# Kernel tuning notes

Measured on AMD Instinct MI355X. Metric: run time of the kernel, lower is better.

The kernel has to match this reference:

```python
import jax, jax.numpy as jnp
import numpy as np

N = 2000      # batch_size * num_rois
PS = 7        # pool_size
C = 256       # roi-align channels
HID = 1024    # head width
NC = 81       # num_classes (COCO incl. background)
EPS = 1e-3    # keras BatchNormalization default epsilon


def setup_inputs() -> dict:
    key = jax.random.key(0)
    ks = jax.random.split(key, 6)
    sc = lambda k, shape, s: jax.random.normal(k, shape, jnp.float32) * s
    return {
        "pooled_rois": jax.random.normal(ks[0], (N, PS, PS, C), jnp.float32),
        # 7x7 VALID conv on a 7x7 input == flattened dense: [PS*PS*C, HID]
        "w1": sc(ks[1], (PS * PS * C, HID), 0.01),
        "b1": jnp.zeros((HID,), jnp.float32),
        "gamma1": jnp.ones((HID,), jnp.float32),
        "beta1": jnp.zeros((HID,), jnp.float32),
        # 1x1 conv == dense [HID, HID]
        "w2": sc(ks[2], (HID, HID), 0.02),
        "b2": jnp.zeros((HID,), jnp.float32),
        "gamma2": jnp.ones((HID,), jnp.float32),
        "beta2": jnp.zeros((HID,), jnp.float32),
        "w_logits": sc(ks[3], (HID, NC), 0.02),
        "b_logits": jnp.zeros((NC,), jnp.float32),
        "w_delta": sc(ks[4], (HID, NC * 4), 0.02),
        "b_delta": jnp.zeros((NC * 4,), jnp.float32),
    }


def _batchnorm_train(x, gamma, beta):
    # training=True: normalize with batch statistics over the RoI axis
    mu = jnp.mean(x, axis=0)
    var = jnp.var(x, axis=0)
    return gamma * (x - mu) * jax.lax.rsqrt(var + EPS) + beta


def reference(pooled_rois, w1, b1, gamma1, beta1, w2, b2, gamma2, beta2,
              w_logits, b_logits, w_delta, b_delta):
    n = pooled_rois.shape[0]
    # rcnn_class_conv1: 7x7 VALID conv on 7x7 input -> flatten + matmul
    x = pooled_rois.reshape(n, -1) @ w1 + b1          # [N, 1024]
    x = jax.nn.relu(_batchnorm_train(x, gamma1, beta1))
    # rcnn_class_conv2: 1x1 conv -> matmul
    x = x @ w2 + b2                                    # [N, 1024]
    x = jax.nn.relu(_batchnorm_train(x, gamma2, beta2))
    logits = x @ w_logits + b_logits                   # [N, NC]
    probs = jax.nn.softmax(logits, axis=-1)            # [N, NC]
    deltas = (x @ w_delta + b_delta).reshape(n, NC, 4) # [N, NC, 4]
    return logits, probs, deltas
```

## Files before the change

kernel.cpp:

```cpp
#include <hip/hip_runtime.h>

typedef unsigned short u16;
typedef __bf16 bf16x8 __attribute__((ext_vector_type(8)));
typedef float f32x4 __attribute__((ext_vector_type(4)));
typedef u16 u16x8 __attribute__((ext_vector_type(8)));
typedef u16 u16x4 __attribute__((ext_vector_type(4)));

static constexpr int kNRoi = 2000;
static constexpr int kMPad = 2048;
static constexpr int kKin  = 12544;
static constexpr int kHid  = 1024;
static constexpr int kNOutPad = 512;
static constexpr int kNC = 81;
static constexpr int kND = 324;

__device__ __forceinline__ float bf2f(u16 h) {
  union { unsigned u; float f; } v; v.u = ((unsigned)h) << 16; return v.f;
}
__device__ __forceinline__ u16 f2bf(float f) {
  union { float f; unsigned u; } v; v.f = f;
  unsigned r = v.u + 0x7fffu + ((v.u >> 16) & 1u);
  return (u16)(r >> 16);
}

__global__ void sniff(const void* __restrict__ g, int* __restrict__ flag) {
  *flag = (((const unsigned*)g)[0] == 0x3f800000u) ? 1 : 0;
}

__global__ void to_bf16(const void* __restrict__ in, u16* __restrict__ out,
                        const int* __restrict__ flagp) {
  const int f32 = *flagp;
  long i = ((long)blockIdx.x * blockDim.x + threadIdx.x) * 8;
  u16x8 h;
  if (f32) {
    f32x4 a = *(const f32x4*)((const float*)in + i);
    f32x4 b = *(const f32x4*)((const float*)in + i + 4);
#pragma unroll
    for (int j = 0; j < 4; ++j) { h[j] = f2bf(a[j]); h[4 + j] = f2bf(b[j]); }
  } else {
    h = *(const u16x8*)((const u16*)in + i);
  }
  *(u16x8*)(out + i) = h;
}

__global__ void transpose_fast(const void* __restrict__ in, u16* __restrict__ out,
                               int R, int C, const int* __restrict__ flagp) {
  __shared__ u16 t[64 * 72];
  const int f32 = *flagp;
  const int tid = threadIdx.x;
  const int cb = blockIdx.x * 64, rb = blockIdx.y * 64;
  const int rl = tid >> 4;
  const int cl = (tid & 15) * 4;
#pragma unroll
  for (int i = 0; i < 4; ++i) {
    int r = rl + i * 16;
    long idx = (long)(rb + r) * C + cb + cl;
    u16 h[4];
    if (f32) {
      f32x4 v = *(const f32x4*)((const float*)in + idx);
#pragma unroll
      for (int j = 0; j < 4; ++j) h[j] = f2bf(v[j]);
    } else {
      u16x4 v = *(const u16x4*)((const u16*)in + idx);
#pragma unroll
      for (int j = 0; j < 4; ++j) h[j] = v[j];
    }
#pragma unroll
    for (int j = 0; j < 4; ++j) t[(cl + j) * 72 + r] = h[j];
  }
  __syncthreads();
  const int c2 = tid >> 3;
  const int r2 = (tid & 7) * 8;
#pragma unroll
  for (int i = 0; i < 2; ++i) {
    int c = c2 + i * 32;
    u16x8 v = *(const u16x8*)&t[c * 72 + r2];
    *(u16x8*)(out + (long)(cb + c) * R + rb + r2) = v;
  }
}

__global__ void transpose_any(const void* __restrict__ in, u16* __restrict__ out,
                              int R, int C, const int* __restrict__ flagp) {
  __shared__ u16 t[32][33];
  const int f32 = *flagp;
  int tx = threadIdx.x & 31, ty = threadIdx.x >> 5;
  int cb = blockIdx.x * 32, rb = blockIdx.y * 32;
#pragma unroll
  for (int i = 0; i < 4; ++i) {
    int r = rb + ty + i * 8, c = cb + tx;
    if (r < R && c < C) {
      long idx = (long)r * C + c;
      t[ty + i * 8][tx] = f32 ? f2bf(((const float*)in)[idx]) : ((const u16*)in)[idx];
    }
  }
  __syncthreads();
#pragma unroll
  for (int i = 0; i < 4; ++i) {
    int c = cb + ty + i * 8, r = rb + tx;
    if (c < C && r < R) out[(long)c * R + r] = t[tx][ty + i * 8];
  }
}

__global__ __launch_bounds__(256) void gemm_bt(
    const u16* __restrict__ A, const u16* __restrict__ Bt,
    float* __restrict__ C, int Mreal, int K, int N, int kchunk) {
  __shared__ u16 As[2][128 * 32];
  __shared__ u16 Bs[2][128 * 32];
  const int tid  = threadIdx.x;
  const int lane = tid & 63;
  const int wave = tid >> 6;
  const int wm = (wave >> 1) * 64;
  const int wn = (wave & 1) * 64;

  f32x4 acc[4][4] = {};

  const int r0 = tid >> 2;
  const int kc = (tid & 3) * 8;
  long ar0 = (long)blockIdx.x * 128 + r0;      if (ar0 > Mreal - 1) ar0 = Mreal - 1;
  long ar1 = (long)blockIdx.x * 128 + 64 + r0; if (ar1 > Mreal - 1) ar1 = Mreal - 1;
  const long br0 = (long)blockIdx.y * 128 + r0;
  const long br1 = br0 + 64;

  const int kb = blockIdx.z * kchunk;
  const u16* ag0 = A + ar0 * K + kb + kc;
  const u16* ag1 = A + ar1 * K + kb + kc;
  const u16* bg0 = Bt + br0 * K + kb + kc;
  const u16* bg1 = Bt + br1 * K + kb + kc;

  const int fr = lane & 15;
  const int fq = (lane >> 4) * 8;
  const int iters = kchunk / 32;

#define STAGE(b) do {                                                          \
    u16* al_ = As[b] + wave * 512;                                             \
    u16* bl_ = Bs[b] + wave * 512;                                             \
    __builtin_amdgcn_global_load_lds((const __attribute__((address_space(1))) void*)ag0, \
                                     (__attribute__((address_space(3))) void*)al_, 16, 0, 0); \
    __builtin_amdgcn_global_load_lds((const __attribute__((address_space(1))) void*)ag1, \
                                     (__attribute__((address_space(3))) void*)(al_ + 2048), 16, 0, 0); \
    __builtin_amdgcn_global_load_lds((const __attribute__((address_space(1))) void*)bg0, \
                                     (__attribute__((address_space(3))) void*)bl_, 16, 0, 0); \
    __builtin_amdgcn_global_load_lds((const __attribute__((address_space(1))) void*)bg1, \
                                     (__attribute__((address_space(3))) void*)(bl_ + 2048), 16, 0, 0); \
    ag0 += 32; ag1 += 32; bg0 += 32; bg1 += 32;                                \
  } while (0)

  STAGE(0);
  int buf = 0;
  for (int it = 0; it < iters; ++it) {
    __syncthreads();
    if (it + 1 < iters) STAGE(buf ^ 1);

    const u16* as_ = As[buf];
    const u16* bs_ = Bs[buf];
    bf16x8 afr[4], bfr[4];
#pragma unroll
    for (int i = 0; i < 4; ++i)
      afr[i] = *(const bf16x8*)(as_ + (wm + i * 16 + fr) * 32 + fq);
#pragma unroll
    for (int i = 0; i < 4; ++i)
      bfr[i] = *(const bf16x8*)(bs_ + (wn + i * 16 + fr) * 32 + fq);
#pragma unroll
    for (int mi = 0; mi < 4; ++mi)
#pragma unroll
      for (int ni = 0; ni < 4; ++ni)
        acc[mi][ni] = __builtin_amdgcn_mfma_f32_16x16x32_bf16(afr[mi], bfr[ni], acc[mi][ni], 0, 0, 0);
    buf ^= 1;
  }
#undef STAGE

  const int row0 = blockIdx.x * 128 + wm + (lane >> 4) * 4;
  const int col0 = blockIdx.y * 128 + wn + fr;
#pragma unroll
  for (int mi = 0; mi < 4; ++mi)
#pragma unroll
    for (int ni = 0; ni < 4; ++ni)
#pragma unroll
      for (int e = 0; e < 4; ++e)
        atomicAdd(&C[(long)(row0 + mi * 16 + e) * N + col0 + ni * 16], acc[mi][ni][e]);
}

__global__ void colstats(const float* __restrict__ X, float* __restrict__ S,
                         float* __restrict__ SS, int cols, int chunk) {
  int c = blockIdx.x * blockDim.x + threadIdx.x;
  int r0 = blockIdx.y * chunk;
  float s = 0.f, ss = 0.f;
  for (int r = r0; r < r0 + chunk; ++r) {
    float v = X[(long)r * cols + c];
    s += v; ss += v * v;
  }
  atomicAdd(&S[c], s);
  atomicAdd(&SS[c], ss);
}

__global__ void finalize_stats(const float* __restrict__ S, const float* __restrict__ SS,
                               const void* __restrict__ gamma, const void* __restrict__ beta,
                               float* __restrict__ SV, float* __restrict__ TV,
                               int n, float invN, const int* __restrict__ flagp) {
  const int f32 = *flagp;
  int c = blockIdx.x * blockDim.x + threadIdx.x;
  if (c < n) {
    float g = f32 ? ((const float*)gamma)[c] : bf2f(((const u16*)gamma)[c]);
    float b = f32 ? ((const float*)beta)[c]  : bf2f(((const u16*)beta)[c]);
    float mu = S[c] * invN;
    float var = SS[c] * invN - mu * mu;
    float sc = g * rsqrtf(var + 1e-3f);
    SV[c] = sc;
    TV[c] = b - mu * sc;
  }
}

__global__ void bn_relu_kernel(const float* __restrict__ X, const float* __restrict__ SV,
                               const float* __restrict__ TV, u16* __restrict__ H) {
  long i = ((long)blockIdx.x * blockDim.x + threadIdx.x) * 8;
  int c = (int)(i & (kHid - 1));
  f32x4 x0 = *(const f32x4*)(X + i);
  f32x4 x1 = *(const f32x4*)(X + i + 4);
  f32x4 s0 = *(const f32x4*)(SV + c);
  f32x4 s1 = *(const f32x4*)(SV + c + 4);
  f32x4 t0 = *(const f32x4*)(TV + c);
  f32x4 t1 = *(const f32x4*)(TV + c + 4);
  u16x8 h;
#pragma unroll
  for (int j = 0; j < 4; ++j) {
    h[j]     = f2bf(fmaxf(0.f, s0[j] * x0[j] + t0[j]));
    h[4 + j] = f2bf(fmaxf(0.f, s1[j] * x1[j] + t1[j]));
  }
  *(u16x8*)(H + i) = h;
}

__global__ void head_out(const float* __restrict__ X, const void* __restrict__ blv,
                         const void* __restrict__ bdv, void* __restrict__ outv,
                         const int* __restrict__ flagp) {
  const int f32 = *flagp;
  int lane = threadIdx.x & 63;
  int row = blockIdx.x * 4 + (threadIdx.x >> 6);
  if (row >= kNRoi) return;
  const float* xr = X + (long)row * kNOutPad;
  auto ldb = [&](const void* p, int i) -> float {
    return f32 ? ((const float*)p)[i] : bf2f(((const u16*)p)[i]);
  };
  auto st = [&](long i, float v) {
    if (f32) ((float*)outv)[i] = v; else ((u16*)outv)[i] = f2bf(v);
  };
  float v0 = xr[lane] + ldb(blv, lane);
  float v1 = (lane < kNC - 64) ? xr[64 + lane] + ldb(blv, 64 + lane) : -3.0e38f;
  float m = fmaxf(v0, v1);
#pragma unroll
  for (int off = 32; off > 0; off >>= 1) m = fmaxf(m, __shfl_xor(m, off, 64));
  float e0 = __expf(v0 - m);
  float e1 = (lane < kNC - 64) ? __expf(v1 - m) : 0.f;
  float s = e0 + e1;
#pragma unroll
  for (int off = 32; off > 0; off >>= 1) s += __shfl_xor(s, off, 64);
  float inv = 1.f / s;
  long lo = (long)row * kNC;
  long pr = (long)kNRoi * kNC + lo;
  long de = 2L * kNRoi * kNC + (long)row * kND;
  st(lo + lane, v0);
  st(pr + lane, e0 * inv);
  if (lane < kNC - 64) { st(lo + 64 + lane, v1); st(pr + 64 + lane, e1 * inv); }
#pragma unroll
  for (int j = 0; j < 5; ++j) {
    int c = lane + 64 * j;
    st(de + c, xr[kNC + c] + ldb(bdv, c));
  }
  if (lane < 4) { int c = lane + 320; st(de + c, xr[kNC + c] + ldb(bdv, c)); }
}

extern "C" void kernel_launch(void* const* d_in, const int* in_sizes, int n_in,
                              void* d_out, int out_size, void* d_ws, size_t ws_size,
                              hipStream_t stream) {
  const void* pooled   = d_in[0];
  const void* w1       = d_in[1];
  const void* gamma1   = d_in[3];
  const void* beta1    = d_in[4];
  const void* w2       = d_in[5];
  const void* gamma2   = d_in[7];
  const void* beta2    = d_in[8];
  const void* w_logits = d_in[9];
  const void* b_logits = d_in[10];
  const void* w_delta  = d_in[11];
  const void* b_delta  = d_in[12];

  char* ws = (char*)d_ws;
  u16*   W1T  = (u16*)(ws + 0);
  u16*   W2T  = (u16*)(ws + 25690112);
  u16*   WHT  = (u16*)(ws + 27787264);
  float* BUFA = (float*)(ws + 28835840);
  u16*   BUFB = (u16*)(ws + 37224448);
  float* S    = (float*)(ws + 41418752);
  float* SS   = S + 1024;
  float* SV   = S + 2048;
  float* TV   = S + 3072;
  int*   FLAG = (int*)(S + 4096);
  u16*   A1   = (u16*)(ws + 41451520);

  const float invN = 1.f / (float)kNRoi;

  sniff<<<1, 1, 0, stream>>>(gamma1, FLAG);

  to_bf16<<<12250, 256, 0, stream>>>(pooled, A1, FLAG);

  hipMemsetAsync(WHT, 0, (size_t)kNOutPad * kHid * sizeof(u16), stream);
  transpose_fast<<<dim3(16, 196), 256, 0, stream>>>(w1, W1T, kKin, kHid, FLAG);
  transpose_fast<<<dim3(16, 16),  256, 0, stream>>>(w2, W2T, kHid, kHid, FLAG);
  transpose_any<<<dim3(3, 32),   256, 0, stream>>>(w_logits, WHT, kHid, kNC, FLAG);
  transpose_any<<<dim3(11, 32),  256, 0, stream>>>(w_delta, WHT + (long)kNC * kHid, kHid, kND, FLAG);

  hipMemsetAsync(BUFA, 0, (size_t)kMPad * kHid * sizeof(float), stream);
  gemm_bt<<<dim3(16, 8, 8), 256, 0, stream>>>(A1, W1T, BUFA, kNRoi, kKin, kHid, kKin / 8);

  hipMemsetAsync(S, 0, 2 * kHid * sizeof(float), stream);
  colstats<<<dim3(kHid / 256, 80), 256, 0, stream>>>(BUFA, S, SS, kHid, kNRoi / 80);
  finalize_stats<<<kHid / 256, 256, 0, stream>>>(S, SS, gamma1, beta1, SV, TV, kHid, invN, FLAG);
  bn_relu_kernel<<<(kMPad * kHid) / (256 * 8), 256, 0, stream>>>(BUFA, SV, TV, BUFB);

  hipMemsetAsync(BUFA, 0, (size_t)kMPad * kHid * sizeof(float), stream);
  gemm_bt<<<dim3(16, 8, 2), 256, 0, stream>>>(BUFB, W2T, BUFA, kMPad, kHid, kHid, kHid / 2);

  hipMemsetAsync(S, 0, 2 * kHid * sizeof(float), stream);
  colstats<<<dim3(kHid / 256, 80), 256, 0, stream>>>(BUFA, S, SS, kHid, kNRoi / 80);
  finalize_stats<<<kHid / 256, 256, 0, stream>>>(S, SS, gamma2, beta2, SV, TV, kHid, invN, FLAG);
  bn_relu_kernel<<<(kMPad * kHid) / (256 * 8), 256, 0, stream>>>(BUFA, SV, TV, BUFB);

  hipMemsetAsync(BUFA, 0, (size_t)kMPad * kNOutPad * sizeof(float), stream);
  gemm_bt<<<dim3(16, 4, 4), 256, 0, stream>>>(BUFB, WHT, BUFA, kMPad, kHid, kNOutPad, kHid / 4);

  head_out<<<kNRoi / 4, 256, 0, stream>>>(BUFA, b_logits, b_delta, d_out, FLAG);
}
```

Before: 428.6 us.

## Fuse prep, zeroing and BN finalize kernels; drop dtype sniffing and memsets

All input conversion and weight transposes, plus zeroing of the accumulation buffers and stats, are merged into one prep kernel dispatched by block index. Zeroing of the second-layer and head output buffers is folded into the colstats kernel, and the BN scale/shift finalize is recomputed inline inside bn_relu. The runtime f32/bf16 sniff is removed and inputs are assumed to be f32. Split-K for the second GEMM goes from 2 to 4. The aim is to cut launch and memset overhead, at the cost of redundant per-element rsqrt work and more atomic traffic in GEMM2.

```diff
diff --git a/kernel.cpp b/kernel.cpp
--- a/kernel.cpp
+++ b/kernel.cpp
@@ -4,7 +4,6 @@
 typedef __bf16 bf16x8 __attribute__((ext_vector_type(8)));
 typedef float f32x4 __attribute__((ext_vector_type(4)));
 typedef u16 u16x8 __attribute__((ext_vector_type(8)));
-typedef u16 u16x4 __attribute__((ext_vector_type(4)));
 
 static constexpr int kNRoi = 2000;
 static constexpr int kMPad = 2048;
@@ -14,63 +13,27 @@
 static constexpr int kNC = 81;
 static constexpr int kND = 324;
 
-__device__ __forceinline__ float bf2f(u16 h) {
-  union { unsigned u; float f; } v; v.u = ((unsigned)h) << 16; return v.f;
-}
+
 __device__ __forceinline__ u16 f2bf(float f) {
   union { float f; unsigned u; } v; v.f = f;
   unsigned r = v.u + 0x7fffu + ((v.u >> 16) & 1u);
   return (u16)(r >> 16);
 }
 
-__global__ void sniff(const void* __restrict__ g, int* __restrict__ flag) {
-  *flag = (((const unsigned*)g)[0] == 0x3f800000u) ? 1 : 0;
-}
-
-__global__ void to_bf16(const void* __restrict__ in, u16* __restrict__ out,
-                        const int* __restrict__ flagp) {
-  const int f32 = *flagp;
-  long i = ((long)blockIdx.x * blockDim.x + threadIdx.x) * 8;
-  u16x8 h;
-  if (f32) {
-    f32x4 a = *(const f32x4*)((const float*)in + i);
-    f32x4 b = *(const f32x4*)((const float*)in + i + 4);
-#pragma unroll
-    for (int j = 0; j < 4; ++j) { h[j] = f2bf(a[j]); h[4 + j] = f2bf(b[j]); }
-  } else {
-    h = *(const u16x8*)((const u16*)in + i);
-  }
-  *(u16x8*)(out + i) = h;
-}
-
-__global__ void transpose_fast(const void* __restrict__ in, u16* __restrict__ out,
-                               int R, int C, const int* __restrict__ flagp) {
-  __shared__ u16 t[64 * 72];
-  const int f32 = *flagp;
-  const int tid = threadIdx.x;
-  const int cb = blockIdx.x * 64, rb = blockIdx.y * 64;
-  const int rl = tid >> 4;
-  const int cl = (tid & 15) * 4;
+__device__ __forceinline__ void transpose64(const float* __restrict__ in,
+                                            u16* __restrict__ out, int R, int C,
+                                            int bx, int by, u16* t, int tid) {
+  const int cb = bx * 64, rb = by * 64;
+  const int rl = tid >> 4, cl = (tid & 15) * 4;
 #pragma unroll
   for (int i = 0; i < 4; ++i) {
     int r = rl + i * 16;
-    long idx = (long)(rb + r) * C + cb + cl;
-    u16 h[4];
-    if (f32) {
-      f32x4 v = *(const f32x4*)((const float*)in + idx);
-#pragma unroll
-      for (int j = 0; j < 4; ++j) h[j] = f2bf(v[j]);
-    } else {
-      u16x4 v = *(const u16x4*)((const u16*)in + idx);
-#pragma unroll
-      for (int j = 0; j < 4; ++j) h[j] = v[j];
-    }
-#pragma unroll
-    for (int j = 0; j < 4; ++j) t[(cl + j) * 72 + r] = h[j];
+    f32x4 v = *(const f32x4*)(in + (long)(rb + r) * C + cb + cl);
+#pragma unroll
+    for (int j = 0; j < 4; ++j) t[(cl + j) * 72 + r] = f2bf(v[j]);
   }
   __syncthreads();
-  const int c2 = tid >> 3;
-  const int r2 = (tid & 7) * 8;
+  const int c2 = tid >> 3, r2 = (tid & 7) * 8;
 #pragma unroll
   for (int i = 0; i < 2; ++i) {
     int c = c2 + i * 32;
@@ -79,26 +42,64 @@
   }
 }
 
-__global__ void transpose_any(const void* __restrict__ in, u16* __restrict__ out,
-                              int R, int C, const int* __restrict__ flagp) {
-  __shared__ u16 t[32][33];
-  const int f32 = *flagp;
-  int tx = threadIdx.x & 31, ty = threadIdx.x >> 5;
-  int cb = blockIdx.x * 32, rb = blockIdx.y * 32;
+__device__ __forceinline__ void transpose32(const float* __restrict__ in,
+                                            u16* __restrict__ out, int R, int C,
+                                            int bx, int by, u16* t, int tid) {
+  int tx = tid & 31, ty = tid >> 5;
+  int cb = bx * 32, rb = by * 32;
 #pragma unroll
   for (int i = 0; i < 4; ++i) {
     int r = rb + ty + i * 8, c = cb + tx;
-    if (r < R && c < C) {
-      long idx = (long)r * C + c;
-      t[ty + i * 8][tx] = f32 ? f2bf(((const float*)in)[idx]) : ((const u16*)in)[idx];
-    }
+    if (r < R && c < C) t[(ty + i * 8) * 33 + tx] = f2bf(in[(long)r * C + c]);
   }
   __syncthreads();
 #pragma unroll
   for (int i = 0; i < 4; ++i) {
     int c = cb + ty + i * 8, r = rb + tx;
-    if (c < C && r < R) out[(long)c * R + r] = t[tx][ty + i * 8];
-  }
+    if (c < C && r < R) out[(long)c * R + r] = t[tx * 33 + ty + i * 8];
+  }
+}
+
+__global__ __launch_bounds__(256) void prep(
+    const float* __restrict__ pooled, const float* __restrict__ w1,
+    const float* __restrict__ w2, const float* __restrict__ wl,
+    const float* __restrict__ wd, u16* __restrict__ A1,
+    u16* __restrict__ W1T, u16* __restrict__ W2T, u16* __restrict__ WHT,
+    float* __restrict__ X1, float* __restrict__ S) {
+  __shared__ u16 sh[64 * 72];
+  const int tid = threadIdx.x;
+  int id = blockIdx.x;
+  if (id < 12250) {
+    long i = ((long)id * 256 + tid) * 8;
+    f32x4 a = *(const f32x4*)(pooled + i);
+    f32x4 b = *(const f32x4*)(pooled + i + 4);
+    u16x8 h;
+#pragma unroll
+    for (int j = 0; j < 4; ++j) { h[j] = f2bf(a[j]); h[4 + j] = f2bf(b[j]); }
+    *(u16x8*)(A1 + i) = h;
+    return;
+  }
+  id -= 12250;
+  if (id < 3136) { transpose64(w1, W1T, kKin, kHid, id & 15, id >> 4, sh, tid); return; }
+  id -= 3136;
+  if (id < 256)  { transpose64(w2, W2T, kHid, kHid, id & 15, id >> 4, sh, tid); return; }
+  id -= 256;
+  if (id < 96)   { transpose32(wl, WHT, kHid, kNC, id % 3, id / 3, sh, tid); return; }
+  id -= 96;
+  if (id < 352)  { transpose32(wd, WHT + kNC * kHid, kHid, kND, id % 11, id / 11, sh, tid); return; }
+  id -= 352;
+  if (id < 54) {
+    int idx = id * 256 + tid;
+    if (idx < 13696) *(u16x8*)(WHT + 405 * kHid + idx * 8) = (u16x8){};
+    return;
+  }
+  id -= 54;
+  if (id < 2048) {
+    *(f32x4*)(X1 + ((long)id * 256 + tid) * 4) = (f32x4){};
+    return;
+  }
+  id -= 2048;
+  *(f32x4*)(S + ((long)id * 256 + tid) * 4) = (f32x4){};
 }
 
 __global__ __launch_bounds__(256) void gemm_bt(
@@ -180,71 +181,63 @@
         atomicAdd(&C[(long)(row0 + mi * 16 + e) * N + col0 + ni * 16], acc[mi][ni][e]);
 }
 
-__global__ void colstats(const float* __restrict__ X, float* __restrict__ S,
-                         float* __restrict__ SS, int cols, int chunk) {
-  int c = blockIdx.x * blockDim.x + threadIdx.x;
-  int r0 = blockIdx.y * chunk;
-  float s = 0.f, ss = 0.f;
-  for (int r = r0; r < r0 + chunk; ++r) {
-    float v = X[(long)r * cols + c];
-    s += v; ss += v * v;
-  }
-  atomicAdd(&S[c], s);
-  atomicAdd(&SS[c], ss);
-}
-
-__global__ void finalize_stats(const float* __restrict__ S, const float* __restrict__ SS,
-                               const void* __restrict__ gamma, const void* __restrict__ beta,
-                               float* __restrict__ SV, float* __restrict__ TV,
-                               int n, float invN, const int* __restrict__ flagp) {
-  const int f32 = *flagp;
-  int c = blockIdx.x * blockDim.x + threadIdx.x;
-  if (c < n) {
-    float g = f32 ? ((const float*)gamma)[c] : bf2f(((const u16*)gamma)[c]);
-    float b = f32 ? ((const float*)beta)[c]  : bf2f(((const u16*)beta)[c]);
-    float mu = S[c] * invN;
-    float var = SS[c] * invN - mu * mu;
-    float sc = g * rsqrtf(var + 1e-3f);
-    SV[c] = sc;
-    TV[c] = b - mu * sc;
-  }
-}
-
-__global__ void bn_relu_kernel(const float* __restrict__ X, const float* __restrict__ SV,
-                               const float* __restrict__ TV, u16* __restrict__ H) {
-  long i = ((long)blockIdx.x * blockDim.x + threadIdx.x) * 8;
+__global__ __launch_bounds__(256) void colstats_zero(
+    const float* __restrict__ X, float* __restrict__ S, float* __restrict__ SS,
+    float* __restrict__ Z) {
+  int id = blockIdx.x;
+  if (id < 320) {
+    int c = (id & 3) * 256 + threadIdx.x;
+    int r0 = (id >> 2) * 25;
+    float s = 0.f, ss = 0.f;
+    for (int r = r0; r < r0 + 25; ++r) {
+      float v = X[(long)r * kHid + c];
+      s += v; ss += v * v;
+    }
+    atomicAdd(&S[c], s);
+    atomicAdd(&SS[c], ss);
+  } else {
+    id -= 320;
+    *(f32x4*)(Z + ((long)id * 256 + threadIdx.x) * 4) = (f32x4){};
+  }
+}
+
+__global__ __launch_bounds__(256) void bn_relu(
+    const float* __restrict__ X, const float* __restrict__ S,
+    const float* __restrict__ SS, const float* __restrict__ gamma,
+    const float* __restrict__ beta, u16* __restrict__ H) {
+  constexpr float invN = 1.f / (float)kNRoi;
+  long i = ((long)blockIdx.x * 256 + threadIdx.x) * 8;
   int c = (int)(i & (kHid - 1));
   f32x4 x0 = *(const f32x4*)(X + i);
   f32x4 x1 = *(const f32x4*)(X + i + 4);
-  f32x4 s0 = *(const f32x4*)(SV + c);
-  f32x4 s1 = *(const f32x4*)(SV + c + 4);
-  f32x4 t0 = *(const f32x4*)(TV + c);
-  f32x4 t1 = *(const f32x4*)(TV + c + 4);
+  f32x4 s0 = *(const f32x4*)(S + c),    s1 = *(const f32x4*)(S + c + 4);
+  f32x4 q0 = *(const f32x4*)(SS + c),   q1 = *(const f32x4*)(SS + c + 4);
+  f32x4 g0 = *(const f32x4*)(gamma + c), g1 = *(const f32x4*)(gamma + c + 4);
+  f32x4 b0 = *(const f32x4*)(beta + c),  b1 = *(const f32x4*)(beta + c + 4);
   u16x8 h;
 #pragma unroll
   for (int j = 0; j < 4; ++j) {
-    h[j]     = f2bf(fmaxf(0.f, s0[j] * x0[j] + t0[j]));
-    h[4 + j] = f2bf(fmaxf(0.f, s1[j] * x1[j] + t1[j]));
+    float mu = s0[j] * invN;
+    float var = q0[j] * invN - mu * mu;
+    float sc = g0[j] * rsqrtf(var + 1e-3f);
+    h[j] = f2bf(fmaxf(0.f, sc * x0[j] + (b0[j] - mu * sc)));
+    mu = s1[j] * invN;
+    var = q1[j] * invN - mu * mu;
+    sc = g1[j] * rsqrtf(var + 1e-3f);
+    h[4 + j] = f2bf(fmaxf(0.f, sc * x1[j] + (b1[j] - mu * sc)));
   }
   *(u16x8*)(H + i) = h;
 }
 
-__global__ void head_out(const float* __restrict__ X, const void* __restrict__ blv,
-                         const void* __restrict__ bdv, void* __restrict__ outv,
-                         const int* __restrict__ flagp) {
-  const int f32 = *flagp;
+__global__ __launch_bounds__(256) void head_out(
+    const float* __restrict__ X, const float* __restrict__ bl,
+    const float* __restrict__ bd, float* __restrict__ out) {
   int lane = threadIdx.x & 63;
   int row = blockIdx.x * 4 + (threadIdx.x >> 6);
   if (row >= kNRoi) return;
   const float* xr = X + (long)row * kNOutPad;
-  auto ldb = [&](const void* p, int i) -> float {
-    return f32 ? ((const float*)p)[i] : bf2f(((const u16*)p)[i]);
-  };
-  auto st = [&](long i, float v) {
-    if (f32) ((float*)outv)[i] = v; else ((u16*)outv)[i] = f2bf(v);
-  };
-  float v0 = xr[lane] + ldb(blv, lane);
-  float v1 = (lane < kNC - 64) ? xr[64 + lane] + ldb(blv, 64 + lane) : -3.0e38f;
+  float v0 = xr[lane] + bl[lane];
+  float v1 = (lane < kNC - 64) ? xr[64 + lane] + bl[64 + lane] : -3.0e38f;
   float m = fmaxf(v0, v1);
 #pragma unroll
   for (int off = 32; off > 0; off >>= 1) m = fmaxf(m, __shfl_xor(m, off, 64));
@@ -254,78 +247,65 @@
 #pragma unroll
   for (int off = 32; off > 0; off >>= 1) s += __shfl_xor(s, off, 64);
   float inv = 1.f / s;
-  long lo = (long)row * kNC;
-  long pr = (long)kNRoi * kNC + lo;
-  long de = 2L * kNRoi * kNC + (long)row * kND;
-  st(lo + lane, v0);
-  st(pr + lane, e0 * inv);
-  if (lane < kNC - 64) { st(lo + 64 + lane, v1); st(pr + 64 + lane, e1 * inv); }
+  float* lo = out + (long)row * kNC;
+  float* pr = out + (long)kNRoi * kNC + (long)row * kNC;
+  float* de = out + 2L * kNRoi * kNC + (long)row * kND;
+  lo[lane] = v0;
+  pr[lane] = e0 * inv;
+  if (lane < kNC - 64) { lo[64 + lane] = v1; pr[64 + lane] = e1 * inv; }
 #pragma unroll
   for (int j = 0; j < 5; ++j) {
     int c = lane + 64 * j;
-    st(de + c, xr[kNC + c] + ldb(bdv, c));
-  }
-  if (lane < 4) { int c = lane + 320; st(de + c, xr[kNC + c] + ldb(bdv, c)); }
+    de[c] = xr[kNC + c] + bd[c];
+  }
+  if (lane < 4) { int c = lane + 320; de[c] = xr[kNC + c] + bd[c]; }
 }
 
 extern "C" void kernel_launch(void* const* d_in, const int* in_sizes, int n_in,
                               void* d_out, int out_size, void* d_ws, size_t ws_size,
                               hipStream_t stream) {
-  const void* pooled   = d_in[0];
-  const void* w1       = d_in[1];
-  const void* gamma1   = d_in[3];
-  const void* beta1    = d_in[4];
-  const void* w2       = d_in[5];
-  const void* gamma2   = d_in[7];
-  const void* beta2    = d_in[8];
-  const void* w_logits = d_in[9];
-  const void* b_logits = d_in[10];
-  const void* w_delta  = d_in[11];
-  const void* b_delta  = d_in[12];
+  const float* pooled   = (const float*)d_in[0];
+  const float* w1       = (const float*)d_in[1];
+  const float* gamma1   = (const float*)d_in[3];
+  const float* beta1    = (const float*)d_in[4];
+  const float* w2       = (const float*)d_in[5];
+  const float* gamma2   = (const float*)d_in[7];
+  const float* beta2    = (const float*)d_in[8];
+  const float* w_logits = (const float*)d_in[9];
+  const float* b_logits = (const float*)d_in[10];
+  const float* w_delta  = (const float*)d_in[11];
+  const float* b_delta  = (const float*)d_in[12];
 
   char* ws = (char*)d_ws;
   u16*   W1T  = (u16*)(ws + 0);
   u16*   W2T  = (u16*)(ws + 25690112);
   u16*   WHT  = (u16*)(ws + 27787264);
-  float* BUFA = (float*)(ws + 28835840);
-  u16*   BUFB = (u16*)(ws + 37224448);
+  float* X1   = (float*)(ws + 28835840);
+  u16*   H    = (u16*)(ws + 37224448);
   float* S    = (float*)(ws + 41418752);
-  float* SS   = S + 1024;
-  float* SV   = S + 2048;
-  float* TV   = S + 3072;
-  int*   FLAG = (int*)(S + 4096);
-  u16*   A1   = (u16*)(ws + 41451520);
-
-  const float invN = 1.f / (float)kNRoi;
-
-  sniff<<<1, 1, 0, stream>>>(gamma1, FLAG);
-
-  to_bf16<<<12250, 256, 0, stream>>>(pooled, A1, FLAG);
-
-  hipMemsetAsync(WHT, 0, (size_t)kNOutPad * kHid * sizeof(u16), stream);
-  transpose_fast<<<dim3(16, 196), 256, 0, stream>>>(w1, W1T, kKin, kHid, FLAG);
-  transpose_fast<<<dim3(16, 16),  256, 0, stream>>>(w2, W2T, kHid, kHid, FLAG);
-  transpose_any<<<dim3(3, 32),   256, 0, stream>>>(w_logits, WHT, kHid, kNC, FLAG);
-  transpose_any<<<dim3(11, 32),  256, 0, stream>>>(w_delta, WHT + (long)kNC * kHid, kHid, kND, FLAG);
-
-  hipMemsetAsync(BUFA, 0, (size_t)kMPad * kHid * sizeof(float), stream);
-  gemm_bt<<<dim3(16, 8, 8), 256, 0, stream>>>(A1, W1T, BUFA, kNRoi, kKin, kHid, kKin / 8);
-
-  hipMemsetAsync(S, 0, 2 * kHid * sizeof(float), stream);
-  colstats<<<dim3(kHid / 256, 80), 256, 0, stream>>>(BUFA, S, SS, kHid, kNRoi / 80);
-  finalize_stats<<<kHid / 256, 256, 0, stream>>>(S, SS, gamma1, beta1, SV, TV, kHid, invN, FLAG);
-  bn_relu_kernel<<<(kMPad * kHid) / (256 * 8), 256, 0, stream>>>(BUFA, SV, TV, BUFB);
-
-  hipMemsetAsync(BUFA, 0, (size_t)kMPad * kHid * sizeof(float), stream);
-  gemm_bt<<<dim3(16, 8, 2), 256, 0, stream>>>(BUFB, W2T, BUFA, kMPad, kHid, kHid, kHid / 2);
-
-  hipMemsetAsync(S, 0, 2 * kHid * sizeof(float), stream);
-  colstats<<<dim3(kHid / 256, 80), 256, 0, stream>>>(BUFA, S, SS, kHid, kNRoi / 80);
-  finalize_stats<<<kHid / 256, 256, 0, stream>>>(S, SS, gamma2, beta2, SV, TV, kHid, invN, FLAG);
-  bn_relu_kernel<<<(kMPad * kHid) / (256 * 8), 256, 0, stream>>>(BUFA, SV, TV, BUFB);
-
-  hipMemsetAsync(BUFA, 0, (size_t)kMPad * kNOutPad * sizeof(float), stream);
-  gemm_bt<<<dim3(16, 4, 4), 256, 0, stream>>>(BUFB, WHT, BUFA, kMPad, kHid, kNOutPad, kHid / 4);
-
-  head_out<<<kNRoi / 4, 256, 0, stream>>>(BUFA, b_logits, b_delta, d_out, FLAG);
-}
+  u16*   A1   = (u16*)(ws + 41435136);
+  float* X2   = (float*)(ws + 41435136);
+  float* XOUT = (float*)(ws + 49823744);
+
+  float* S1  = S;
+  float* SS1 = S + 1024;
+  float* S2  = S + 2048;
+  float* SS2 = S + 3072;
+
+  prep<<<18196, 256, 0, stream>>>(pooled, w1, w2, w_logits, w_delta,
+                                  A1, W1T, W2T, WHT, X1, S);
+
+  gemm_bt<<<dim3(16, 8, 8), 256, 0, stream>>>(A1, W1T, X1, kNRoi, kKin, kHid, kKin / 8);
+
+  colstats_zero<<<320 + 3072, 256, 0, stream>>>(X1, S1, SS1, X2);
+  bn_relu<<<(kMPad * kHid) / 2048, 256, 0, stream>>>(X1, S1, SS1, gamma1, beta1, H);
+
+  gemm_bt<<<dim3(16, 8, 4), 256, 0, stream>>>(H, W2T, X2, kMPad, kHid, kHid, kHid / 4);
+
+  colstats_zero<<<320, 256, 0, stream>>>(X2, S2, SS2, nullptr);
+  bn_relu<<<(kMPad * kHid) / 2048, 256, 0, stream>>>(X2, S2, SS2, gamma2, beta2, H);
+
+  gemm_bt<<<dim3(16, 4, 4), 256, 0, stream>>>(H, WHT, XOUT, kMPad, kHid, kNOutPad, kHid / 4);
+
+  head_out<<<kNRoi / 4, 256, 0, stream>>>(XOUT, b_logits, b_delta, (float*)d_out);
+}
```

Result: faster. 387.6 us (-9.6%).
